# Optimization experiments

Measured on AMD Instinct MI355X. Metric: run time of the kernel, lower is better.

The kernel has to match this reference:

```python
import jax, jax.numpy as jnp
import numpy as np

N_IN = 100000
N_OUT = 200000
C_IN = 128
C_OUT = 64
K = 27  # 3x3x3 kernel offsets
M = 100000  # neighbor-map pairs per kernel offset
BN_EPS = 1e-5


def setup_inputs() -> dict:
    key = jax.random.key(0)
    k1, k2, k3, k4 = jax.random.split(key, 4)
    x = jax.random.normal(k1, (N_IN, C_IN), dtype=jnp.float32)
    weight = jax.random.normal(k2, (K, C_IN, C_OUT), dtype=jnp.float32) * (1.0 / np.sqrt(C_IN * K))
    gamma = jnp.ones((C_OUT,), dtype=jnp.float32)
    beta = jnp.zeros((C_OUT,), dtype=jnp.float32)
    in_map = jax.random.randint(k3, (K, M), 0, N_IN, dtype=jnp.int32)
    out_map = jax.random.randint(k4, (K, M), 0, N_OUT, dtype=jnp.int32)
    return {"x": x, "weight": weight, "gamma": gamma, "beta": beta,
            "in_map": in_map, "out_map": out_map}


def sparse_transposed_conv(x, weight, in_map, out_map):
    # gather-GEMM-scatter over K kernel offsets (torchsparse semantics)
    out = jnp.zeros((N_OUT, C_OUT), dtype=x.dtype)

    def body(k, out):
        gathered = x[in_map[k]]                # [M, C_in] irregular gather
        contrib = gathered @ weight[k]         # [M, C_out] small GEMM
        return out.at[out_map[k]].add(contrib) # irregular scatter-add

    return jax.lax.fori_loop(0, K, body, out)


def reference(x, weight, gamma, beta, in_map, out_map):
    out = sparse_transposed_conv(x, weight, in_map, out_map)
    # BatchNorm over points (training-mode batch statistics, biased var)
    mean = jnp.mean(out, axis=0)
    var = jnp.mean(jnp.square(out - mean), axis=0)
    y = (out - mean) * (gamma * jax.lax.rsqrt(var + BN_EPS)) + beta
    return jnp.maximum(y, 0.0)  # ReLU
```

## Files before the change

### kernel.cpp

```cpp
#include <hip/hip_runtime.h>
#include <hip/hip_fp16.h>

#define N_IN   100000
#define N_OUT  200000
#define C_IN   128
#define C_OUT  64
#define NK     27
#define MM     100000
#define BN_EPS 1e-5f

#define TILE_M 128
#define APAD   136

typedef short bf16x8 __attribute__((ext_vector_type(8)));
typedef float f32x4  __attribute__((ext_vector_type(4)));

__device__ __forceinline__ unsigned pack2_bf16(float a, float b) {
  unsigned ua = __float_as_uint(a);
  unsigned ub = __float_as_uint(b);
  ua = (ua + 0x7FFFu + ((ua >> 16) & 1u)) >> 16;
  ub = (ub + 0x7FFFu + ((ub >> 16) & 1u)) & 0xFFFF0000u;
  return ua | ub;
}

__device__ __forceinline__ unsigned pack2_f16(float lo, float hi) {
  __half2 h = __floats2half2_rn(lo, hi);
  return *(unsigned*)&h;
}

__device__ __forceinline__ void pk_atomic_f16(const void* addr, unsigned pw) {
  asm volatile("global_atomic_pk_add_f16 %0, %1, off"
               :: "v"((unsigned long long)addr), "v"(pw) : "memory");
}

__global__ void convert_wt_kernel(const float* __restrict__ w, unsigned* __restrict__ wt) {
  int pidx = blockIdx.x * 256 + threadIdx.x;
  int k   = pidx >> 12;
  int rem = pidx & 4095;
  int co  = rem >> 6;
  int ci0 = (rem & 63) * 2;
  const float* wk = w + (size_t)k * C_IN * C_OUT;
  float a = wk[ci0 * C_OUT + co];
  float b = wk[(ci0 + 1) * C_OUT + co];
  wt[pidx] = pack2_bf16(a, b);
}

template <bool F16>
__global__ __launch_bounds__(256) void scatter_kernel(
    const float* __restrict__ x,
    const unsigned short* __restrict__ wt,
    const int* __restrict__ in_map,
    const int* __restrict__ out_map,
    float* __restrict__ outf,
    unsigned short* __restrict__ acc16)
{
  __shared__ unsigned short Als[TILE_M * APAD];
  __shared__ unsigned short Bls[C_OUT * APAD];
  __shared__ int om[TILE_M];

  const int t = threadIdx.x;
  const int k = blockIdx.y;
  const int mbase = blockIdx.x * TILE_M;

  if (t < TILE_M) {
    int m = mbase + t;
    om[t] = (m < MM) ? out_map[k * MM + m] : 0;
  }

  {
    const uint4* src = (const uint4*)(wt + (size_t)k * C_OUT * C_IN);
    #pragma unroll
    for (int i = 0; i < 4; ++i) {
      int ch  = t + i * 256;
      int co  = ch >> 4;
      int ci0 = (ch & 15) * 8;
      *(uint4*)&Bls[co * APAD + ci0] = src[ch];
    }
  }

  {
    int r    = t >> 1;
    int half = t & 1;
    int m    = mbase + r;
    int src  = (m < MM) ? in_map[k * MM + m] : 0;
    const float4* xr = (const float4*)(x + (size_t)src * C_IN) + half * 16;
    uint2* dst = (uint2*)&Als[r * APAD + half * 64];
    #pragma unroll
    for (int j = 0; j < 16; ++j) {
      float4 v = xr[j];
      dst[j] = make_uint2(pack2_bf16(v.x, v.y), pack2_bf16(v.z, v.w));
    }
  }
  __syncthreads();

  const int wave = t >> 6;
  const int lane = t & 63;
  const int quad = lane >> 4;
  const int l15  = lane & 15;
  const int rb   = wave * 32;

  f32x4 acc[2][4];
  #pragma unroll
  for (int i = 0; i < 2; ++i)
    #pragma unroll
    for (int j = 0; j < 4; ++j)
      acc[i][j] = (f32x4){0.f, 0.f, 0.f, 0.f};

  #pragma unroll
  for (int kk = 0; kk < 4; ++kk) {
    const int koff = kk * 32 + quad * 8;
    bf16x8 a0 = *(const bf16x8*)&Als[(rb + l15) * APAD + koff];
    bf16x8 a1 = *(const bf16x8*)&Als[(rb + 16 + l15) * APAD + koff];
    bf16x8 b0 = *(const bf16x8*)&Bls[(l15) * APAD + koff];
    bf16x8 b1 = *(const bf16x8*)&Bls[(16 + l15) * APAD + koff];
    bf16x8 b2 = *(const bf16x8*)&Bls[(32 + l15) * APAD + koff];
    bf16x8 b3 = *(const bf16x8*)&Bls[(48 + l15) * APAD + koff];
    acc[0][0] = __builtin_amdgcn_mfma_f32_16x16x32_bf16(a0, b0, acc[0][0], 0, 0, 0);
    acc[0][1] = __builtin_amdgcn_mfma_f32_16x16x32_bf16(a0, b1, acc[0][1], 0, 0, 0);
    acc[0][2] = __builtin_amdgcn_mfma_f32_16x16x32_bf16(a0, b2, acc[0][2], 0, 0, 0);
    acc[0][3] = __builtin_amdgcn_mfma_f32_16x16x32_bf16(a0, b3, acc[0][3], 0, 0, 0);
    acc[1][0] = __builtin_amdgcn_mfma_f32_16x16x32_bf16(a1, b0, acc[1][0], 0, 0, 0);
    acc[1][1] = __builtin_amdgcn_mfma_f32_16x16x32_bf16(a1, b1, acc[1][1], 0, 0, 0);
    acc[1][2] = __builtin_amdgcn_mfma_f32_16x16x32_bf16(a1, b2, acc[1][2], 0, 0, 0);
    acc[1][3] = __builtin_amdgcn_mfma_f32_16x16x32_bf16(a1, b3, acc[1][3], 0, 0, 0);
  }

  if constexpr (F16) {
    const int par = l15 & 1;
    #pragma unroll
    for (int rt = 0; rt < 2; ++rt) {
      int rloc = rb + rt * 16 + quad * 4;
      int mrow = mbase + rloc;
      #pragma unroll
      for (int ct = 0; ct < 4; ++ct) {
        f32x4 v = acc[rt][ct];
        int colb = ct * 16 + (l15 & ~1);
        #pragma unroll
        for (int i = 0; i < 4; ++i) {
          float vn = __shfl_xor(v[i], 1);
          float lo = par ? vn : v[i];
          float hi = par ? v[i] : vn;
          unsigned pw = pack2_f16(lo, hi);
          if (((i & 1) == par) && (mrow + i < MM)) {
            const unsigned short* addr = acc16 + (size_t)om[rloc + i] * C_OUT + colb;
            pk_atomic_f16(addr, pw);
          }
        }
      }
    }
  } else {
    #pragma unroll
    for (int rt = 0; rt < 2; ++rt) {
      int rloc = rb + rt * 16 + quad * 4;
      int4 o4 = *(const int4*)&om[rloc];
      int mrow = mbase + rloc;
      #pragma unroll
      for (int ct = 0; ct < 4; ++ct) {
        f32x4 v = acc[rt][ct];
        int col = ct * 16 + l15;
        if (mrow + 0 < MM) unsafeAtomicAdd(&outf[(size_t)o4.x * C_OUT + col], v[0]);
        if (mrow + 1 < MM) unsafeAtomicAdd(&outf[(size_t)o4.y * C_OUT + col], v[1]);
        if (mrow + 2 < MM) unsafeAtomicAdd(&outf[(size_t)o4.z * C_OUT + col], v[2]);
        if (mrow + 3 < MM) unsafeAtomicAdd(&outf[(size_t)o4.w * C_OUT + col], v[3]);
      }
    }
  }
}

__global__ __launch_bounds__(256) void stats16_kernel(const unsigned* __restrict__ acc,
                                                      float* __restrict__ ws) {
  __shared__ float red[4][8][32];
  int t = threadIdx.x;
  int w = t & 31, sub = t >> 5;
  float s0 = 0, q0 = 0, s1 = 0, q1 = 0;
  for (int r = blockIdx.x * 8 + sub; r < N_OUT; r += gridDim.x * 8) {
    unsigned u = acc[(size_t)r * 32 + w];
    __half2 h = *(__half2*)&u;
    float a = __low2float(h), b = __high2float(h);
    s0 += a; q0 += a * a; s1 += b; q1 += b * b;
  }
  red[0][sub][w] = s0; red[1][sub][w] = q0;
  red[2][sub][w] = s1; red[3][sub][w] = q1;
  __syncthreads();
  if (t < 32) {
    float S0 = 0, Q0 = 0, S1 = 0, Q1 = 0;
    #pragma unroll
    for (int s = 0; s < 8; ++s) {
      S0 += red[0][s][t]; Q0 += red[1][s][t];
      S1 += red[2][s][t]; Q1 += red[3][s][t];
    }
    unsafeAtomicAdd(&ws[2 * t],      S0);
    unsafeAtomicAdd(&ws[64 + 2 * t], Q0);
    unsafeAtomicAdd(&ws[2 * t + 1],      S1);
    unsafeAtomicAdd(&ws[64 + 2 * t + 1], Q1);
  }
}

__global__ void finalize16_kernel(const uint2* __restrict__ acc,
                                  float* __restrict__ out,
                                  const float* __restrict__ ws) {
  int i = blockIdx.x * 256 + threadIdx.x;
  uint2 u = acc[i];
  __half2 h0 = *(__half2*)&u.x;
  __half2 h1 = *(__half2*)&u.y;
  int c0 = (i & 15) * 4;
  float s0 = ws[128 + c0], s1 = ws[129 + c0], s2 = ws[130 + c0], s3 = ws[131 + c0];
  float b0 = ws[192 + c0], b1 = ws[193 + c0], b2 = ws[194 + c0], b3 = ws[195 + c0];
  float4 v;
  v.x = fmaxf(fmaf(__low2float(h0),  s0, b0), 0.f);
  v.y = fmaxf(fmaf(__high2float(h0), s1, b1), 0.f);
  v.z = fmaxf(fmaf(__low2float(h1),  s2, b2), 0.f);
  v.w = fmaxf(fmaf(__high2float(h1), s3, b3), 0.f);
  ((float4*)out)[i] = v;
}

__global__ void stats_kernel(const float* __restrict__ out, float* __restrict__ ws) {
  __shared__ float ls[4][64];
  __shared__ float ls2[4][64];
  int t = threadIdx.x;
  int c = t & 63, sub = t >> 6;
  float s = 0.f, s2 = 0.f;
  for (int r = blockIdx.x * 4 + sub; r < N_OUT; r += gridDim.x * 4) {
    float v = out[(size_t)r * C_OUT + c];
    s += v; s2 += v * v;
  }
  ls[sub][c] = s; ls2[sub][c] = s2;
  __syncthreads();
  if (t < 64) {
    float ts = ls[0][t] + ls[1][t] + ls[2][t] + ls[3][t];
    float t2 = ls2[0][t] + ls2[1][t] + ls2[2][t] + ls2[3][t];
    unsafeAtomicAdd(&ws[t], ts);
    unsafeAtomicAdd(&ws[64 + t], t2);
  }
}

__global__ void finalize_kernel(float* __restrict__ out, const float* __restrict__ ws) {
  int i = blockIdx.x * 256 + threadIdx.x;
  float4 v = ((const float4*)out)[i];
  int c0 = (i & 15) * 4;
  float s0 = ws[128 + c0], s1 = ws[129 + c0], s2 = ws[130 + c0], s3 = ws[131 + c0];
  float b0 = ws[192 + c0], b1 = ws[193 + c0], b2 = ws[194 + c0], b3 = ws[195 + c0];
  v.x = fmaxf(fmaf(v.x, s0, b0), 0.f);
  v.y = fmaxf(fmaf(v.y, s1, b1), 0.f);
  v.z = fmaxf(fmaf(v.z, s2, b2), 0.f);
  v.w = fmaxf(fmaf(v.w, s3, b3), 0.f);
  ((float4*)out)[i] = v;
}

__global__ void prep_kernel(float* __restrict__ ws,
                            const float* __restrict__ gamma,
                            const float* __restrict__ beta) {
  int c = threadIdx.x;
  float mean = ws[c] * (1.0f / N_OUT);
  float var  = ws[64 + c] * (1.0f / N_OUT) - mean * mean;
  var = fmaxf(var, 0.0f);
  float sc = gamma[c] * rsqrtf(var + BN_EPS);
  ws[128 + c] = sc;
  ws[192 + c] = beta[c] - mean * sc;
}

extern "C" void kernel_launch(void* const* d_in, const int* in_sizes, int n_in,
                              void* d_out, int out_size, void* d_ws, size_t ws_size,
                              hipStream_t stream) {
  const float* x      = (const float*)d_in[0];
  const float* weight = (const float*)d_in[1];
  const float* gamma  = (const float*)d_in[2];
  const float* beta   = (const float*)d_in[3];
  const int* in_map   = (const int*)d_in[4];
  const int* out_map  = (const int*)d_in[5];
  float* out   = (float*)d_out;
  float* stats = (float*)d_ws;
  unsigned* wt = (unsigned*)((char*)d_ws + 1024);
  unsigned short* acc16 = (unsigned short*)((char*)d_ws + (1 << 20));

  const size_t ACC_BYTES = (size_t)N_OUT * C_OUT * sizeof(unsigned short);
  const bool f16path = ws_size >= ((1u << 20) + ACC_BYTES);

  hipMemsetAsync(d_ws, 0, 1024, stream);
  convert_wt_kernel<<<432, 256, 0, stream>>>(weight, wt);

  dim3 g((MM + TILE_M - 1) / TILE_M, NK);
  if (f16path) {
    hipMemsetAsync(acc16, 0, ACC_BYTES, stream);
    scatter_kernel<true><<<g, 256, 0, stream>>>(x, (const unsigned short*)wt,
                                                in_map, out_map, out, acc16);
    stats16_kernel<<<1024, 256, 0, stream>>>((const unsigned*)acc16, stats);
    prep_kernel<<<1, 64, 0, stream>>>(stats, gamma, beta);
    finalize16_kernel<<<(N_OUT * C_OUT / 4 + 255) / 256, 256, 0, stream>>>(
        (const uint2*)acc16, out, stats);
  } else {
    hipMemsetAsync(d_out, 0, (size_t)N_OUT * C_OUT * sizeof(float), stream);
    scatter_kernel<false><<<g, 256, 0, stream>>>(x, (const unsigned short*)wt,
                                                 in_map, out_map, out, acc16);
    stats_kernel<<<512, 256, 0, stream>>>(out, stats);
    prep_kernel<<<1, 64, 0, stream>>>(stats, gamma, beta);
    finalize_kernel<<<(N_OUT * C_OUT / 4 + 255) / 256, 256, 0, stream>>>(out, stats);
  }
}
```

Baseline: 750.7 us.

## Pre-convert x to bf16 and gather A fragments directly into registers

Adds a conversion pass that turns x into bf16 once, so the scatter kernel gathers half as many bytes per row. The new scatter kernel loads each lane's MFMA A-fragment straight from global memory into registers. This drops the A tile in LDS and one staging step, and lets the kernel target higher occupancy through launch_bounds(256,4). Out_map values are now read straight from global memory in the epilogue. The cost is an extra full pass over x each call, and the fallback path converts x without ever using it. In the fallback, the bf16 copy may also be written past a small workspace.

After: 732.8 us. -2.4%, faster.

```diff
diff --git a/kernel.cpp b/kernel.cpp
--- a/kernel.cpp
+++ b/kernel.cpp
@@ -33,39 +33,44 @@
                :: "v"((unsigned long long)addr), "v"(pw) : "memory");
 }
 
-__global__ void convert_wt_kernel(const float* __restrict__ w, unsigned* __restrict__ wt) {
-  int pidx = blockIdx.x * 256 + threadIdx.x;
-  int k   = pidx >> 12;
-  int rem = pidx & 4095;
-  int co  = rem >> 6;
-  int ci0 = (rem & 63) * 2;
-  const float* wk = w + (size_t)k * C_IN * C_OUT;
-  float a = wk[ci0 * C_OUT + co];
-  float b = wk[(ci0 + 1) * C_OUT + co];
-  wt[pidx] = pack2_bf16(a, b);
-}
-
-template <bool F16>
-__global__ __launch_bounds__(256) void scatter_kernel(
-    const float* __restrict__ x,
+__global__ void convert_kernel(const float* __restrict__ x, unsigned* __restrict__ xb,
+                               const float* __restrict__ w, unsigned* __restrict__ wt) {
+  if (blockIdx.x < 6250) {
+    int id = blockIdx.x * 256 + threadIdx.x;
+    const float4* xs = (const float4*)x;
+    float4 v0 = xs[2 * id];
+    float4 v1 = xs[2 * id + 1];
+    uint4 o;
+    o.x = pack2_bf16(v0.x, v0.y);
+    o.y = pack2_bf16(v0.z, v0.w);
+    o.z = pack2_bf16(v1.x, v1.y);
+    o.w = pack2_bf16(v1.z, v1.w);
+    ((uint4*)xb)[id] = o;
+  } else {
+    int pidx = (blockIdx.x - 6250) * 256 + threadIdx.x;
+    int k   = pidx >> 12;
+    int rem = pidx & 4095;
+    int co  = rem >> 6;
+    int ci0 = (rem & 63) * 2;
+    const float* wk = w + (size_t)k * C_IN * C_OUT;
+    float a = wk[ci0 * C_OUT + co];
+    float b = wk[(ci0 + 1) * C_OUT + co];
+    wt[pidx] = pack2_bf16(a, b);
+  }
+}
+
+__global__ __launch_bounds__(256, 4) void scatter3_kernel(
+    const uint4* __restrict__ xb,
     const unsigned short* __restrict__ wt,
     const int* __restrict__ in_map,
     const int* __restrict__ out_map,
-    float* __restrict__ outf,
     unsigned short* __restrict__ acc16)
 {
-  __shared__ unsigned short Als[TILE_M * APAD];
   __shared__ unsigned short Bls[C_OUT * APAD];
-  __shared__ int om[TILE_M];
 
   const int t = threadIdx.x;
   const int k = blockIdx.y;
   const int mbase = blockIdx.x * TILE_M;
-
-  if (t < TILE_M) {
-    int m = mbase + t;
-    om[t] = (m < MM) ? out_map[k * MM + m] : 0;
-  }
 
   {
     const uint4* src = (const uint4*)(wt + (size_t)k * C_OUT * C_IN);
@@ -78,6 +83,116 @@
     }
   }
 
+  const int wave = t >> 6;
+  const int lane = t & 63;
+  const int quad = lane >> 4;
+  const int l15  = lane & 15;
+  const int rb   = wave * 32;
+
+  const int m0 = mbase + rb + l15;
+  const int m1 = m0 + 16;
+  const int src0 = (m0 < MM) ? in_map[k * MM + m0] : 0;
+  const int src1 = (m1 < MM) ? in_map[k * MM + m1] : 0;
+  const uint4* xr0 = xb + (size_t)src0 * 16 + quad;
+  const uint4* xr1 = xb + (size_t)src1 * 16 + quad;
+  uint4 a0[4], a1[4];
+  #pragma unroll
+  for (int kk = 0; kk < 4; ++kk) {
+    a0[kk] = xr0[kk * 4];
+    a1[kk] = xr1[kk * 4];
+  }
+
+  __syncthreads();
+
+  f32x4 acc[2][4];
+  #pragma unroll
+  for (int i = 0; i < 2; ++i)
+    #pragma unroll
+    for (int j = 0; j < 4; ++j)
+      acc[i][j] = (f32x4){0.f, 0.f, 0.f, 0.f};
+
+  #pragma unroll
+  for (int kk = 0; kk < 4; ++kk) {
+    const int koff = kk * 32 + quad * 8;
+    bf16x8 fa0 = *(const bf16x8*)&a0[kk];
+    bf16x8 fa1 = *(const bf16x8*)&a1[kk];
+    bf16x8 b0 = *(const bf16x8*)&Bls[(l15) * APAD + koff];
+    bf16x8 b1 = *(const bf16x8*)&Bls[(16 + l15) * APAD + koff];
+    bf16x8 b2 = *(const bf16x8*)&Bls[(32 + l15) * APAD + koff];
+    bf16x8 b3 = *(const bf16x8*)&Bls[(48 + l15) * APAD + koff];
+    acc[0][0] = __builtin_amdgcn_mfma_f32_16x16x32_bf16(fa0, b0, acc[0][0], 0, 0, 0);
+    acc[0][1] = __builtin_amdgcn_mfma_f32_16x16x32_bf16(fa0, b1, acc[0][1], 0, 0, 0);
+    acc[0][2] = __builtin_amdgcn_mfma_f32_16x16x32_bf16(fa0, b2, acc[0][2], 0, 0, 0);
+    acc[0][3] = __builtin_amdgcn_mfma_f32_16x16x32_bf16(fa0, b3, acc[0][3], 0, 0, 0);
+    acc[1][0] = __builtin_amdgcn_mfma_f32_16x16x32_bf16(fa1, b0, acc[1][0], 0, 0, 0);
+    acc[1][1] = __builtin_amdgcn_mfma_f32_16x16x32_bf16(fa1, b1, acc[1][1], 0, 0, 0);
+    acc[1][2] = __builtin_amdgcn_mfma_f32_16x16x32_bf16(fa1, b2, acc[1][2], 0, 0, 0);
+    acc[1][3] = __builtin_amdgcn_mfma_f32_16x16x32_bf16(fa1, b3, acc[1][3], 0, 0, 0);
+  }
+
+  const int par = l15 & 1;
+  #pragma unroll
+  for (int rt = 0; rt < 2; ++rt) {
+    int rloc = rb + rt * 16 + quad * 4;
+    int mrow = mbase + rloc;
+    int4 o4;
+    if (mrow + 3 < MM) {
+      o4 = *(const int4*)(out_map + (size_t)k * MM + mrow);
+    } else {
+      o4.x = (mrow + 0 < MM) ? out_map[(size_t)k * MM + mrow + 0] : 0;
+      o4.y = (mrow + 1 < MM) ? out_map[(size_t)k * MM + mrow + 1] : 0;
+      o4.z = (mrow + 2 < MM) ? out_map[(size_t)k * MM + mrow + 2] : 0;
+      o4.w = (mrow + 3 < MM) ? out_map[(size_t)k * MM + mrow + 3] : 0;
+    }
+    int om4[4] = {o4.x, o4.y, o4.z, o4.w};
+    #pragma unroll
+    for (int ct = 0; ct < 4; ++ct) {
+      f32x4 v = acc[rt][ct];
+      int colb = ct * 16 + (l15 & ~1);
+      #pragma unroll
+      for (int i = 0; i < 4; ++i) {
+        float vn = __shfl_xor(v[i], 1);
+        float lo = par ? vn : v[i];
+        float hi = par ? v[i] : vn;
+        unsigned pw = pack2_f16(lo, hi);
+        if (((i & 1) == par) && (mrow + i < MM)) {
+          const unsigned short* addr = acc16 + (size_t)om4[i] * C_OUT + colb;
+          pk_atomic_f16(addr, pw);
+        }
+      }
+    }
+  }
+}
+
+__global__ __launch_bounds__(256) void scatter_f32_kernel(
+    const float* __restrict__ x,
+    const unsigned short* __restrict__ wt,
+    const int* __restrict__ in_map,
+    const int* __restrict__ out_map,
+    float* __restrict__ outf)
+{
+  __shared__ unsigned short Als[TILE_M * APAD];
+  __shared__ unsigned short Bls[C_OUT * APAD];
+  __shared__ int om[TILE_M];
+
+  const int t = threadIdx.x;
+  const int k = blockIdx.y;
+  const int mbase = blockIdx.x * TILE_M;
+
+  if (t < TILE_M) {
+    int m = mbase + t;
+    om[t] = (m < MM) ? out_map[k * MM + m] : 0;
+  }
+  {
+    const uint4* src = (const uint4*)(wt + (size_t)k * C_OUT * C_IN);
+    #pragma unroll
+    for (int i = 0; i < 4; ++i) {
+      int ch  = t + i * 256;
+      int co  = ch >> 4;
+      int ci0 = (ch & 15) * 8;
+      *(uint4*)&Bls[co * APAD + ci0] = src[ch];
+    }
+  }
   {
     int r    = t >> 1;
     int half = t & 1;
@@ -125,44 +240,19 @@
     acc[1][3] = __builtin_amdgcn_mfma_f32_16x16x32_bf16(a1, b3, acc[1][3], 0, 0, 0);
   }
 
-  if constexpr (F16) {
-    const int par = l15 & 1;
-    #pragma unroll
-    for (int rt = 0; rt < 2; ++rt) {
-      int rloc = rb + rt * 16 + quad * 4;
-      int mrow = mbase + rloc;
-      #pragma unroll
-      for (int ct = 0; ct < 4; ++ct) {
-        f32x4 v = acc[rt][ct];
-        int colb = ct * 16 + (l15 & ~1);
-        #pragma unroll
-        for (int i = 0; i < 4; ++i) {
-          float vn = __shfl_xor(v[i], 1);
-          float lo = par ? vn : v[i];
-          float hi = par ? v[i] : vn;
-          unsigned pw = pack2_f16(lo, hi);
-          if (((i & 1) == par) && (mrow + i < MM)) {
-            const unsigned short* addr = acc16 + (size_t)om[rloc + i] * C_OUT + colb;
-            pk_atomic_f16(addr, pw);
-          }
-        }
-      }
-    }
-  } else {
-    #pragma unroll
-    for (int rt = 0; rt < 2; ++rt) {
-      int rloc = rb + rt * 16 + quad * 4;
-      int4 o4 = *(const int4*)&om[rloc];
-      int mrow = mbase + rloc;
-      #pragma unroll
-      for (int ct = 0; ct < 4; ++ct) {
-        f32x4 v = acc[rt][ct];
-        int col = ct * 16 + l15;
-        if (mrow + 0 < MM) unsafeAtomicAdd(&outf[(size_t)o4.x * C_OUT + col], v[0]);
-        if (mrow + 1 < MM) unsafeAtomicAdd(&outf[(size_t)o4.y * C_OUT + col], v[1]);
-        if (mrow + 2 < MM) unsafeAtomicAdd(&outf[(size_t)o4.z * C_OUT + col], v[2]);
-        if (mrow + 3 < MM) unsafeAtomicAdd(&outf[(size_t)o4.w * C_OUT + col], v[3]);
-      }
+  #pragma unroll
+  for (int rt = 0; rt < 2; ++rt) {
+    int rloc = rb + rt * 16 + quad * 4;
+    int4 o4 = *(const int4*)&om[rloc];
+    int mrow = mbase + rloc;
+    #pragma unroll
+    for (int ct = 0; ct < 4; ++ct) {
+      f32x4 v = acc[rt][ct];
+      int col = ct * 16 + l15;
+      if (mrow + 0 < MM) unsafeAtomicAdd(&outf[(size_t)o4.x * C_OUT + col], v[0]);
+      if (mrow + 1 < MM) unsafeAtomicAdd(&outf[(size_t)o4.y * C_OUT + col], v[1]);
+      if (mrow + 2 < MM) unsafeAtomicAdd(&outf[(size_t)o4.z * C_OUT + col], v[2]);
+      if (mrow + 3 < MM) unsafeAtomicAdd(&outf[(size_t)o4.w * C_OUT + col], v[3]);
     }
   }
 }
@@ -270,28 +360,34 @@
   const int* out_map  = (const int*)d_in[5];
   float* out   = (float*)d_out;
   float* stats = (float*)d_ws;
-  unsigned* wt = (unsigned*)((char*)d_ws + 1024);
-  unsigned short* acc16 = (unsigned short*)((char*)d_ws + (1 << 20));
-
-  const size_t ACC_BYTES = (size_t)N_OUT * C_OUT * sizeof(unsigned short);
-  const bool f16path = ws_size >= ((1u << 20) + ACC_BYTES);
-
+
+  const size_t WT_OFF  = 4096;
+  const size_t XB_OFF  = 1u << 20;
+  const size_t XB_SZ   = (size_t)N_IN * C_IN * 2;
+  const size_t ACC_OFF = XB_OFF + XB_SZ;
+  const size_t ACC_SZ  = (size_t)N_OUT * C_OUT * 2;
+
+  unsigned* wt = (unsigned*)((char*)d_ws + WT_OFF);
+  unsigned* xb = (unsigned*)((char*)d_ws + XB_OFF);
+  unsigned short* acc16 = (unsigned short*)((char*)d_ws + ACC_OFF);
+
+  dim3 g((MM + TILE_M - 1) / TILE_M, NK);
   hipMemsetAsync(d_ws, 0, 1024, stream);
-  convert_wt_kernel<<<432, 256, 0, stream>>>(weight, wt);
-
-  dim3 g((MM + TILE_M - 1) / TILE_M, NK);
-  if (f16path) {
-    hipMemsetAsync(acc16, 0, ACC_BYTES, stream);
-    scatter_kernel<true><<<g, 256, 0, stream>>>(x, (const unsigned short*)wt,
-                                                in_map, out_map, out, acc16);
+
+  if (ws_size >= ACC_OFF + ACC_SZ) {
+    hipMemsetAsync(acc16, 0, ACC_SZ, stream);
+    convert_kernel<<<6682, 256, 0, stream>>>(x, xb, weight, wt);
+    scatter3_kernel<<<g, 256, 0, stream>>>((const uint4*)xb, (const unsigned short*)wt,
+                                           in_map, out_map, acc16);
     stats16_kernel<<<1024, 256, 0, stream>>>((const unsigned*)acc16, stats);
     prep_kernel<<<1, 64, 0, stream>>>(stats, gamma, beta);
     finalize16_kernel<<<(N_OUT * C_OUT / 4 + 255) / 256, 256, 0, stream>>>(
         (const uint2*)acc16, out, stats);
   } else {
     hipMemsetAsync(d_out, 0, (size_t)N_OUT * C_OUT * sizeof(float), stream);
-    scatter_kernel<false><<<g, 256, 0, stream>>>(x, (const unsigned short*)wt,
-                                                 in_map, out_map, out, acc16);
+    convert_kernel<<<6682, 256, 0, stream>>>(x, xb, weight, wt);
+    scatter_f32_kernel<<<g, 256, 0, stream>>>(x, (const unsigned short*)wt,
+                                              in_map, out_map, out);
     stats_kernel<<<512, 256, 0, stream>>>(out, stats);
     prep_kernel<<<1, 64, 0, stream>>>(stats, gamma, beta);
     finalize_kernel<<<(N_OUT * C_OUT / 4 + 255) / 256, 256, 0, stream>>>(out, stats);
```

## Pre-convert x to bf16 and gather A fragments directly into registers with prefetch

Applied to the files above, without the earlier changes.

Adds a pre-pass that converts all of x to bf16 once, so the scatter kernel gathers half the bytes per row and skips per-gather conversion. The scatter kernel drops the A shared-memory tile: each wave loads its MFMA A fragments straight from global memory into registers. Each block walks 16 consecutive 64-row tiles and software-prefetches the next tile's indices and rows while computing the current one. The fp32 fallback path is removed, so the kernel now assumes a workspace of roughly 28MB plus the f16 accumulator.

New measurement: 739.4 us. No clear change (-1.5%).

```diff
diff --git a/kernel.cpp b/kernel.cpp
--- a/kernel.cpp
+++ b/kernel.cpp
@@ -9,8 +9,9 @@
 #define MM     100000
 #define BN_EPS 1e-5f
 
-#define TILE_M 128
 #define APAD   136
+#define TM     64
+#define TPB    16
 
 typedef short bf16x8 __attribute__((ext_vector_type(8)));
 typedef float f32x4  __attribute__((ext_vector_type(4)));
@@ -33,39 +34,43 @@
                :: "v"((unsigned long long)addr), "v"(pw) : "memory");
 }
 
-__global__ void convert_wt_kernel(const float* __restrict__ w, unsigned* __restrict__ wt) {
-  int pidx = blockIdx.x * 256 + threadIdx.x;
-  int k   = pidx >> 12;
-  int rem = pidx & 4095;
-  int co  = rem >> 6;
-  int ci0 = (rem & 63) * 2;
-  const float* wk = w + (size_t)k * C_IN * C_OUT;
-  float a = wk[ci0 * C_OUT + co];
-  float b = wk[(ci0 + 1) * C_OUT + co];
-  wt[pidx] = pack2_bf16(a, b);
-}
-
-template <bool F16>
-__global__ __launch_bounds__(256) void scatter_kernel(
-    const float* __restrict__ x,
+__global__ void convert_kernel(const float* __restrict__ x, unsigned* __restrict__ xb,
+                               const float* __restrict__ w, unsigned* __restrict__ wt) {
+  if (blockIdx.x < 6250) {
+    int id = blockIdx.x * 256 + threadIdx.x;
+    const float4* xs = (const float4*)x;
+    float4 v0 = xs[2 * id];
+    float4 v1 = xs[2 * id + 1];
+    uint4 o;
+    o.x = pack2_bf16(v0.x, v0.y);
+    o.y = pack2_bf16(v0.z, v0.w);
+    o.z = pack2_bf16(v1.x, v1.y);
+    o.w = pack2_bf16(v1.z, v1.w);
+    ((uint4*)xb)[id] = o;
+  } else {
+    int pidx = (blockIdx.x - 6250) * 256 + threadIdx.x;
+    int k   = pidx >> 12;
+    int rem = pidx & 4095;
+    int co  = rem >> 6;
+    int ci0 = (rem & 63) * 2;
+    const float* wk = w + (size_t)k * C_IN * C_OUT;
+    float a = wk[ci0 * C_OUT + co];
+    float b = wk[(ci0 + 1) * C_OUT + co];
+    wt[pidx] = pack2_bf16(a, b);
+  }
+}
+
+__global__ __launch_bounds__(256, 4) void scatter6_kernel(
+    const uint4* __restrict__ xb,
     const unsigned short* __restrict__ wt,
     const int* __restrict__ in_map,
     const int* __restrict__ out_map,
-    float* __restrict__ outf,
     unsigned short* __restrict__ acc16)
 {
-  __shared__ unsigned short Als[TILE_M * APAD];
   __shared__ unsigned short Bls[C_OUT * APAD];
-  __shared__ int om[TILE_M];
 
   const int t = threadIdx.x;
   const int k = blockIdx.y;
-  const int mbase = blockIdx.x * TILE_M;
-
-  if (t < TILE_M) {
-    int m = mbase + t;
-    om[t] = (m < MM) ? out_map[k * MM + m] : 0;
-  }
 
   {
     const uint4* src = (const uint4*)(wt + (size_t)k * C_OUT * C_IN);
@@ -77,93 +82,98 @@
       *(uint4*)&Bls[co * APAD + ci0] = src[ch];
     }
   }
-
-  {
-    int r    = t >> 1;
-    int half = t & 1;
-    int m    = mbase + r;
-    int src  = (m < MM) ? in_map[k * MM + m] : 0;
-    const float4* xr = (const float4*)(x + (size_t)src * C_IN) + half * 16;
-    uint2* dst = (uint2*)&Als[r * APAD + half * 64];
-    #pragma unroll
-    for (int j = 0; j < 16; ++j) {
-      float4 v = xr[j];
-      dst[j] = make_uint2(pack2_bf16(v.x, v.y), pack2_bf16(v.z, v.w));
-    }
-  }
   __syncthreads();
 
   const int wave = t >> 6;
   const int lane = t & 63;
   const int quad = lane >> 4;
   const int l15  = lane & 15;
-  const int rb   = wave * 32;
-
-  f32x4 acc[2][4];
-  #pragma unroll
-  for (int i = 0; i < 2; ++i)
-    #pragma unroll
-    for (int j = 0; j < 4; ++j)
-      acc[i][j] = (f32x4){0.f, 0.f, 0.f, 0.f};
-
-  #pragma unroll
-  for (int kk = 0; kk < 4; ++kk) {
-    const int koff = kk * 32 + quad * 8;
-    bf16x8 a0 = *(const bf16x8*)&Als[(rb + l15) * APAD + koff];
-    bf16x8 a1 = *(const bf16x8*)&Als[(rb + 16 + l15) * APAD + koff];
-    bf16x8 b0 = *(const bf16x8*)&Bls[(l15) * APAD + koff];
-    bf16x8 b1 = *(const bf16x8*)&Bls[(16 + l15) * APAD + koff];
-    bf16x8 b2 = *(const bf16x8*)&Bls[(32 + l15) * APAD + koff];
-    bf16x8 b3 = *(const bf16x8*)&Bls[(48 + l15) * APAD + koff];
-    acc[0][0] = __builtin_amdgcn_mfma_f32_16x16x32_bf16(a0, b0, acc[0][0], 0, 0, 0);
-    acc[0][1] = __builtin_amdgcn_mfma_f32_16x16x32_bf16(a0, b1, acc[0][1], 0, 0, 0);
-    acc[0][2] = __builtin_amdgcn_mfma_f32_16x16x32_bf16(a0, b2, acc[0][2], 0, 0, 0);
-    acc[0][3] = __builtin_amdgcn_mfma_f32_16x16x32_bf16(a0, b3, acc[0][3], 0, 0, 0);
-    acc[1][0] = __builtin_amdgcn_mfma_f32_16x16x32_bf16(a1, b0, acc[1][0], 0, 0, 0);
-    acc[1][1] = __builtin_amdgcn_mfma_f32_16x16x32_bf16(a1, b1, acc[1][1], 0, 0, 0);
-    acc[1][2] = __builtin_amdgcn_mfma_f32_16x16x32_bf16(a1, b2, acc[1][2], 0, 0, 0);
-    acc[1][3] = __builtin_amdgcn_mfma_f32_16x16x32_bf16(a1, b3, acc[1][3], 0, 0, 0);
-  }
-
-  if constexpr (F16) {
-    const int par = l15 & 1;
-    #pragma unroll
-    for (int rt = 0; rt < 2; ++rt) {
-      int rloc = rb + rt * 16 + quad * 4;
-      int mrow = mbase + rloc;
+  const int par  = l15 & 1;
+  const int rb16 = wave * 16;
+  const size_t kb = (size_t)k * MM;
+  const int tile0 = blockIdx.x * TPB;
+
+  int mb   = tile0 * TM;
+  int arow = mb + rb16 + l15;
+  int srcr = (arow < MM) ? in_map[kb + arow] : 0;
+  int mrow = mb + rb16 + quad * 4;
+  int4 o4;
+  if (mrow + 3 < MM) {
+    o4 = *(const int4*)(out_map + kb + mrow);
+  } else {
+    o4.x = (mrow + 0 < MM) ? out_map[kb + mrow + 0] : 0;
+    o4.y = (mrow + 1 < MM) ? out_map[kb + mrow + 1] : 0;
+    o4.z = (mrow + 2 < MM) ? out_map[kb + mrow + 2] : 0;
+    o4.w = (mrow + 3 < MM) ? out_map[kb + mrow + 3] : 0;
+  }
+  uint4 a[4];
+  {
+    const uint4* xr = xb + (size_t)srcr * 16 + quad;
+    a[0] = xr[0]; a[1] = xr[4]; a[2] = xr[8]; a[3] = xr[12];
+  }
+
+  for (int j = 0; j < TPB; ++j) {
+    int mb2 = (tile0 + j + 1) * TM;
+    const bool more = (j + 1 < TPB) && (mb2 < MM);
+    int nsrc = 0, nmrow = 0;
+    int4 no4 = make_int4(0, 0, 0, 0);
+    if (more) {
+      int narow = mb2 + rb16 + l15;
+      nsrc  = (narow < MM) ? in_map[kb + narow] : 0;
+      nmrow = mb2 + rb16 + quad * 4;
+      if (nmrow + 3 < MM) {
+        no4 = *(const int4*)(out_map + kb + nmrow);
+      } else {
+        no4.x = (nmrow + 0 < MM) ? out_map[kb + nmrow + 0] : 0;
+        no4.y = (nmrow + 1 < MM) ? out_map[kb + nmrow + 1] : 0;
+        no4.z = (nmrow + 2 < MM) ? out_map[kb + nmrow + 2] : 0;
+        no4.w = (nmrow + 3 < MM) ? out_map[kb + nmrow + 3] : 0;
+      }
+    }
+
+    f32x4 acc[4];
+    #pragma unroll
+    for (int ct = 0; ct < 4; ++ct) acc[ct] = (f32x4){0.f, 0.f, 0.f, 0.f};
+    #pragma unroll
+    for (int kk = 0; kk < 4; ++kk) {
+      const int koff = kk * 32 + quad * 8;
+      bf16x8 fa = *(const bf16x8*)&a[kk];
+      bf16x8 b0 = *(const bf16x8*)&Bls[(l15) * APAD + koff];
+      bf16x8 b1 = *(const bf16x8*)&Bls[(16 + l15) * APAD + koff];
+      bf16x8 b2 = *(const bf16x8*)&Bls[(32 + l15) * APAD + koff];
+      bf16x8 b3 = *(const bf16x8*)&Bls[(48 + l15) * APAD + koff];
+      acc[0] = __builtin_amdgcn_mfma_f32_16x16x32_bf16(fa, b0, acc[0], 0, 0, 0);
+      acc[1] = __builtin_amdgcn_mfma_f32_16x16x32_bf16(fa, b1, acc[1], 0, 0, 0);
+      acc[2] = __builtin_amdgcn_mfma_f32_16x16x32_bf16(fa, b2, acc[2], 0, 0, 0);
+      acc[3] = __builtin_amdgcn_mfma_f32_16x16x32_bf16(fa, b3, acc[3], 0, 0, 0);
+    }
+
+    uint4 na[4];
+    if (more) {
+      const uint4* nxr = xb + (size_t)nsrc * 16 + quad;
+      na[0] = nxr[0]; na[1] = nxr[4]; na[2] = nxr[8]; na[3] = nxr[12];
+    }
+
+    int omv[4] = {o4.x, o4.y, o4.z, o4.w};
+    #pragma unroll
+    for (int ct = 0; ct < 4; ++ct) {
+      f32x4 v = acc[ct];
+      int colb = ct * 16 + (l15 & ~1);
       #pragma unroll
-      for (int ct = 0; ct < 4; ++ct) {
-        f32x4 v = acc[rt][ct];
-        int colb = ct * 16 + (l15 & ~1);
-        #pragma unroll
-        for (int i = 0; i < 4; ++i) {
-          float vn = __shfl_xor(v[i], 1);
-          float lo = par ? vn : v[i];
-          float hi = par ? v[i] : vn;
-          unsigned pw = pack2_f16(lo, hi);
-          if (((i & 1) == par) && (mrow + i < MM)) {
-            const unsigned short* addr = acc16 + (size_t)om[rloc + i] * C_OUT + colb;
-            pk_atomic_f16(addr, pw);
-          }
+      for (int i = 0; i < 4; ++i) {
+        float vn = __shfl_xor(v[i], 1);
+        float lo = par ? vn : v[i];
+        float hi = par ? v[i] : vn;
+        unsigned pw = pack2_f16(lo, hi);
+        if (((i & 1) == par) && (mrow + i < MM)) {
+          pk_atomic_f16(acc16 + (size_t)omv[i] * C_OUT + colb, pw);
         }
       }
     }
-  } else {
-    #pragma unroll
-    for (int rt = 0; rt < 2; ++rt) {
-      int rloc = rb + rt * 16 + quad * 4;
-      int4 o4 = *(const int4*)&om[rloc];
-      int mrow = mbase + rloc;
-      #pragma unroll
-      for (int ct = 0; ct < 4; ++ct) {
-        f32x4 v = acc[rt][ct];
-        int col = ct * 16 + l15;
-        if (mrow + 0 < MM) unsafeAtomicAdd(&outf[(size_t)o4.x * C_OUT + col], v[0]);
-        if (mrow + 1 < MM) unsafeAtomicAdd(&outf[(size_t)o4.y * C_OUT + col], v[1]);
-        if (mrow + 2 < MM) unsafeAtomicAdd(&outf[(size_t)o4.z * C_OUT + col], v[2]);
-        if (mrow + 3 < MM) unsafeAtomicAdd(&outf[(size_t)o4.w * C_OUT + col], v[3]);
-      }
-    }
+
+    if (!more) break;
+    a[0] = na[0]; a[1] = na[1]; a[2] = na[2]; a[3] = na[3];
+    o4 = no4; mrow = nmrow;
   }
 }
 
@@ -194,6 +204,18 @@
     unsafeAtomicAdd(&ws[2 * t + 1],      S1);
     unsafeAtomicAdd(&ws[64 + 2 * t + 1], Q1);
   }
+}
+
+__global__ void prep_kernel(float* __restrict__ ws,
+                            const float* __restrict__ gamma,
+                            const float* __restrict__ beta) {
+  int c = threadIdx.x;
+  float mean = ws[c] * (1.0f / N_OUT);
+  float var  = ws[64 + c] * (1.0f / N_OUT) - mean * mean;
+  var = fmaxf(var, 0.0f);
+  float sc = gamma[c] * rsqrtf(var + BN_EPS);
+  ws[128 + c] = sc;
+  ws[192 + c] = beta[c] - mean * sc;
 }
 
 __global__ void finalize16_kernel(const uint2* __restrict__ acc,
@@ -214,51 +236,6 @@
   ((float4*)out)[i] = v;
 }
 
-__global__ void stats_kernel(const float* __restrict__ out, float* __restrict__ ws) {
-  __shared__ float ls[4][64];
-  __shared__ float ls2[4][64];
-  int t = threadIdx.x;
-  int c = t & 63, sub = t >> 6;
-  float s = 0.f, s2 = 0.f;
-  for (int r = blockIdx.x * 4 + sub; r < N_OUT; r += gridDim.x * 4) {
-    float v = out[(size_t)r * C_OUT + c];
-    s += v; s2 += v * v;
-  }
-  ls[sub][c] = s; ls2[sub][c] = s2;
-  __syncthreads();
-  if (t < 64) {
-    float ts = ls[0][t] + ls[1][t] + ls[2][t] + ls[3][t];
-    float t2 = ls2[0][t] + ls2[1][t] + ls2[2][t] + ls2[3][t];
-    unsafeAtomicAdd(&ws[t], ts);
-    unsafeAtomicAdd(&ws[64 + t], t2);
-  }
-}
-
-__global__ void finalize_kernel(float* __restrict__ out, const float* __restrict__ ws) {
-  int i = blockIdx.x * 256 + threadIdx.x;
-  float4 v = ((const float4*)out)[i];
-  int c0 = (i & 15) * 4;
-  float s0 = ws[128 + c0], s1 = ws[129 + c0], s2 = ws[130 + c0], s3 = ws[131 + c0];
-  float b0 = ws[192 + c0], b1 = ws[193 + c0], b2 = ws[194 + c0], b3 = ws[195 + c0];
-  v.x = fmaxf(fmaf(v.x, s0, b0), 0.f);
-  v.y = fmaxf(fmaf(v.y, s1, b1), 0.f);
-  v.z = fmaxf(fmaf(v.z, s2, b2), 0.f);
-  v.w = fmaxf(fmaf(v.w, s3, b3), 0.f);
-  ((float4*)out)[i] = v;
-}
-
-__global__ void prep_kernel(float* __restrict__ ws,
-                            const float* __restrict__ gamma,
-                            const float* __restrict__ beta) {
-  int c = threadIdx.x;
-  float mean = ws[c] * (1.0f / N_OUT);
-  float var  = ws[64 + c] * (1.0f / N_OUT) - mean * mean;
-  var = fmaxf(var, 0.0f);
-  float sc = gamma[c] * rsqrtf(var + BN_EPS);
-  ws[128 + c] = sc;
-  ws[192 + c] = beta[c] - mean * sc;
-}
-
 extern "C" void kernel_launch(void* const* d_in, const int* in_sizes, int n_in,
                               void* d_out, int out_size, void* d_ws, size_t ws_size,
                               hipStream_t stream) {
@@ -270,30 +247,27 @@
   const int* out_map  = (const int*)d_in[5];
   float* out   = (float*)d_out;
   float* stats = (float*)d_ws;
-  unsigned* wt = (unsigned*)((char*)d_ws + 1024);
-  unsigned short* acc16 = (unsigned short*)((char*)d_ws + (1 << 20));
-
-  const size_t ACC_BYTES = (size_t)N_OUT * C_OUT * sizeof(unsigned short);
-  const bool f16path = ws_size >= ((1u << 20) + ACC_BYTES);
+
+  const size_t WT_OFF  = (size_t)1 << 20;
+  const size_t XB_OFF  = (size_t)2 << 20;
+  const size_t ACC_OFF = (size_t)28 << 20;
+  const size_t ACC_SZ  = (size_t)N_OUT * C_OUT * 2;
+
+  unsigned* wt          = (unsigned*)((char*)d_ws + WT_OFF);
+  unsigned* xb          = (unsigned*)((char*)d_ws + XB_OFF);
+  unsigned short* acc16 = (unsigned short*)((char*)d_ws + ACC_OFF);
 
   hipMemsetAsync(d_ws, 0, 1024, stream);
-  convert_wt_kernel<<<432, 256, 0, stream>>>(weight, wt);
-
-  dim3 g((MM + TILE_M - 1) / TILE_M, NK);
-  if (f16path) {
-    hipMemsetAsync(acc16, 0, ACC_BYTES, stream);
-    scatter_kernel<true><<<g, 256, 0, stream>>>(x, (const unsigned short*)wt,
-                                                in_map, out_map, out, acc16);
-    stats16_kernel<<<1024, 256, 0, stream>>>((const unsigned*)acc16, stats);
-    prep_kernel<<<1, 64, 0, stream>>>(stats, gamma, beta);
-    finalize16_kernel<<<(N_OUT * C_OUT / 4 + 255) / 256, 256, 0, stream>>>(
-        (const uint2*)acc16, out, stats);
-  } else {
-    hipMemsetAsync(d_out, 0, (size_t)N_OUT * C_OUT * sizeof(float), stream);
-    scatter_kernel<false><<<g, 256, 0, stream>>>(x, (const unsigned short*)wt,
-                                                 in_map, out_map, out, acc16);
-    stats_kernel<<<512, 256, 0, stream>>>(out, stats);
-    prep_kernel<<<1, 64, 0, stream>>>(stats, gamma, beta);
-    finalize_kernel<<<(N_OUT * C_OUT / 4 + 255) / 256, 256, 0, stream>>>(out, stats);
-  }
-}
+  hipMemsetAsync(acc16, 0, ACC_SZ, stream);
+
+  convert_kernel<<<6682, 256, 0, stream>>>(x, xb, weight, wt);
+
+  dim3 g((MM + TM * TPB - 1) / (TM * TPB), NK);
+  scatter6_kernel<<<g, 256, 0, stream>>>((const uint4*)xb, (const unsigned short*)wt,
+                                         in_map, out_map, acc16);
+
+  stats16_kernel<<<1024, 256, 0, stream>>>((const unsigned*)acc16, stats);
+  prep_kernel<<<1, 64, 0, stream>>>(stats, gamma, beta);
+  finalize16_kernel<<<(N_OUT * C_OUT / 4) / 256, 256, 0, stream>>>(
+      (const uint2*)acc16, out, stats);
+}
```
